# Kernel tuning notes

Measured on AMD Instinct MI355X. Metric: run time of the kernel, lower is better.

The kernel has to match this reference:

```python
import jax, jax.numpy as jnp
import numpy as np

DIM = 1024
NUM_HEADS = 16
HEAD_DIM = DIM // NUM_HEADS
SCALING = HEAD_DIM ** (-0.5)


def setup_inputs() -> dict:
    key = jax.random.key(0)
    ks = jax.random.split(key, 9)
    B, S = 2, 2048
    s = DIM ** -0.5  # ~ torch Linear init scale
    inp = {
        "x": jax.random.normal(ks[0], (B, S, DIM), dtype=jnp.float32),
        "wq": jax.random.uniform(ks[1], (DIM, DIM), jnp.float32, -s, s),
        "bq": jax.random.uniform(ks[2], (DIM,), jnp.float32, -s, s),
        "wk": jax.random.uniform(ks[3], (DIM, DIM), jnp.float32, -s, s),
        "bk": jax.random.uniform(ks[4], (DIM,), jnp.float32, -s, s),
        "wv": jax.random.uniform(ks[5], (DIM, DIM), jnp.float32, -s, s),
        "bv": jax.random.uniform(ks[6], (DIM,), jnp.float32, -s, s),
        "wo": jax.random.uniform(ks[7], (DIM, DIM), jnp.float32, -s, s),
        "bo": jax.random.uniform(ks[8], (DIM,), jnp.float32, -s, s),
    }
    return inp


def reference(x, wq, bq, wk, bk, wv, bv, wo, bo):
    B, S, D = x.shape
    # projections (weights stored [out,in] like torch Linear -> x @ W.T + b)
    q = (x @ wq.T + bq).reshape(B, S, NUM_HEADS, HEAD_DIM)
    k = (x @ wk.T + bk).reshape(B, S, NUM_HEADS, HEAD_DIM)
    v = (x @ wv.T + bv).reshape(B, S, NUM_HEADS, HEAD_DIM)
    # [B,H,S,S] scores, scaled
    scores = jnp.einsum("bqhd,bkhd->bhqk", q, k) * SCALING
    attn = jax.nn.softmax(scores, axis=-1)
    # dropout p=0.0 (eval): identity
    out = jnp.einsum("bhqk,bkhd->bqhd", attn, v).reshape(B, S, D)
    return out @ wo.T + bo
```

## Files before the change

kernel.cpp:

```cpp
#include <hip/hip_runtime.h>

#define DIM 1024
#define NHEADS 16
#define HDIM 64
#define BATCH 2
#define SEQ 2048
#define MTOT (BATCH*SEQ)
#define QSCALE 0.18033688011112042f
#define XN ((size_t)MTOT*DIM)
#define WN ((size_t)DIM*DIM)

typedef __attribute__((ext_vector_type(8))) short short8;
typedef __attribute__((ext_vector_type(4))) float f32x4;
typedef __attribute__((ext_vector_type(16))) float f32x16;
typedef __attribute__((ext_vector_type(2))) int int2v;

static __device__ __forceinline__ unsigned short bf16rne(float f) {
    unsigned u = __builtin_bit_cast(unsigned, f);
    return (unsigned short)((u + 0x7fffu + ((u >> 16) & 1u)) >> 16);
}

static __device__ __forceinline__ void gld16(const void* g, void* l) {
    __builtin_amdgcn_global_load_lds((const __attribute__((address_space(1))) void*)g,
                                     (__attribute__((address_space(3))) void*)l, 16, 0, 0);
}

__global__ __launch_bounds__(256)
void prep(const float* __restrict__ x, const float* __restrict__ wq, const float* __restrict__ wk,
          const float* __restrict__ wv, const float* __restrict__ wo, unsigned short* __restrict__ dst)
{
    const size_t i = ((size_t)blockIdx.x*256 + threadIdx.x)*8;
    const float* s; size_t o;
    if (i < XN)           { s = x;  o = i; }
    else if (i < XN+WN)   { s = wq; o = i - XN; }
    else if (i < XN+2*WN) { s = wk; o = i - XN - WN; }
    else if (i < XN+3*WN) { s = wv; o = i - XN - 2*WN; }
    else                  { s = wo; o = i - XN - 3*WN; }
    float4 a = *(const float4*)(s + o);
    float4 b = *(const float4*)(s + o + 4);
    uint4 w;
    w.x = (unsigned)bf16rne(a.x) | ((unsigned)bf16rne(a.y) << 16);
    w.y = (unsigned)bf16rne(a.z) | ((unsigned)bf16rne(a.w) << 16);
    w.z = (unsigned)bf16rne(b.x) | ((unsigned)bf16rne(b.y) << 16);
    w.w = (unsigned)bf16rne(b.z) | ((unsigned)bf16rne(b.w) << 16);
    *(uint4*)&dst[i] = w;
}

__global__ __launch_bounds__(256)
void gemm_qkv(const unsigned short* __restrict__ A,
              const unsigned short* __restrict__ W0, const unsigned short* __restrict__ W1,
              const unsigned short* __restrict__ W2,
              const float* __restrict__ b0, const float* __restrict__ b1, const float* __restrict__ b2,
              unsigned short* __restrict__ o0, unsigned short* __restrict__ o1, unsigned short* __restrict__ o2)
{
    __shared__ __align__(16) unsigned short As[2][4096];
    __shared__ __align__(16) unsigned short Bs[2][4096];
    const int t = threadIdx.x, wid = t >> 6, lane = t & 63;
    const int lr = lane & 15, lg = lane >> 4;
    const int bid = blockIdx.y * 24 + blockIdx.x;
    const int swz = (bid & 7) * 96 + (bid >> 3);
    const int sx = swz % 24, sy = swz / 24;
    const int widx = sx >> 3;
    const int n0 = (sx & 7) << 7;
    const int m0 = sy << 7;
    const unsigned short* W = widx == 0 ? W0 : (widx == 1 ? W1 : W2);
    const float* bias        = widx == 0 ? b0 : (widx == 1 ? b1 : b2);
    const float scale        = widx == 0 ? QSCALE : 1.0f;
    unsigned short* out      = widx == 0 ? o0 : (widx == 1 ? o1 : o2);

    const int wm = wid >> 1, wn = wid & 1;
    const int f0 = 2*wid, f1 = f0 + 1;
    const unsigned short* Ag0 = A + (size_t)(m0 + f0*16 + lr)*DIM + lg*8;
    const unsigned short* Ag1 = A + (size_t)(m0 + f1*16 + lr)*DIM + lg*8;
    const unsigned short* Bg0 = W + (size_t)(n0 + f0*16 + lr)*DIM + lg*8;
    const unsigned short* Bg1 = W + (size_t)(n0 + f1*16 + lr)*DIM + lg*8;

    f32x4 acc[4][4] = {};

    gld16(Ag0, &As[0][f0*512]); gld16(Ag1, &As[0][f1*512]);
    gld16(Bg0, &Bs[0][f0*512]); gld16(Bg1, &Bs[0][f1*512]);

    for (int it = 0; it < DIM/32; ++it) {
        __syncthreads();
        {
            const int nbf = (it+1)&1; const int ko = ((it+1)&31)*32;
            gld16(Ag0 + ko, &As[nbf][f0*512]); gld16(Ag1 + ko, &As[nbf][f1*512]);
            gld16(Bg0 + ko, &Bs[nbf][f0*512]); gld16(Bg1 + ko, &Bs[nbf][f1*512]);
        }
        const int cb = it & 1;
        short8 af[4], bf[4];
        #pragma unroll
        for (int i = 0; i < 4; ++i) af[i] = *(const short8*)&As[cb][(wm*4+i)*512 + lane*8];
        #pragma unroll
        for (int i = 0; i < 4; ++i) bf[i] = *(const short8*)&Bs[cb][(wn*4+i)*512 + lane*8];
        __builtin_amdgcn_s_setprio(1);
        #pragma unroll
        for (int mb = 0; mb < 4; ++mb)
            #pragma unroll
            for (int nb = 0; nb < 4; ++nb)
                acc[mb][nb] = __builtin_amdgcn_mfma_f32_16x16x32_bf16(af[mb], bf[nb], acc[mb][nb], 0, 0, 0);
        __builtin_amdgcn_s_setprio(0);
    }

    #pragma unroll
    for (int nb = 0; nb < 4; ++nb) {
        const int col = n0 + wn*64 + nb*16 + lr;
        const float bv = bias[col];
        #pragma unroll
        for (int mb = 0; mb < 4; ++mb) {
            #pragma unroll
            for (int j = 0; j < 4; ++j) {
                const int row = m0 + wm*64 + mb*16 + lg*4 + j;
                out[(size_t)row*DIM + col] = bf16rne((acc[mb][nb][j] + bv) * scale);
            }
        }
    }
}

__global__ __launch_bounds__(256)
void gemm_o(const unsigned short* __restrict__ A, const unsigned short* __restrict__ W,
            const float* __restrict__ bias, float* __restrict__ fo)
{
    __shared__ __align__(16) unsigned short As[2][2048];
    __shared__ __align__(16) unsigned short Bs[2][4096];
    const int t = threadIdx.x, wid = t >> 6, lane = t & 63;
    const int lr = lane & 15, lg = lane >> 4;
    const int bid = blockIdx.y * 8 + blockIdx.x;
    const int swz = (bid & 7) * 64 + (bid >> 3);
    const int n0 = (swz & 7) << 7;
    const int m0 = (swz >> 3) << 6;
    const int wm = wid >> 1, wn = wid & 1;

    const int fa = wid;
    const int g0 = 2*wid, g1 = g0 + 1;
    const unsigned short* Ag  = A + (size_t)(m0 + fa*16 + lr)*DIM + lg*8;
    const unsigned short* Bg0 = W + (size_t)(n0 + g0*16 + lr)*DIM + lg*8;
    const unsigned short* Bg1 = W + (size_t)(n0 + g1*16 + lr)*DIM + lg*8;

    f32x4 acc[2][4] = {};

    gld16(Ag, &As[0][fa*512]);
    gld16(Bg0, &Bs[0][g0*512]); gld16(Bg1, &Bs[0][g1*512]);

    for (int it = 0; it < DIM/32; ++it) {
        __syncthreads();
        {
            const int nbf = (it+1)&1; const int ko = ((it+1)&31)*32;
            gld16(Ag + ko, &As[nbf][fa*512]);
            gld16(Bg0 + ko, &Bs[nbf][g0*512]); gld16(Bg1 + ko, &Bs[nbf][g1*512]);
        }
        const int cb = it & 1;
        short8 af[2], bf[4];
        #pragma unroll
        for (int i = 0; i < 2; ++i) af[i] = *(const short8*)&As[cb][(wm*2+i)*512 + lane*8];
        #pragma unroll
        for (int i = 0; i < 4; ++i) bf[i] = *(const short8*)&Bs[cb][(wn*4+i)*512 + lane*8];
        __builtin_amdgcn_s_setprio(1);
        #pragma unroll
        for (int mb = 0; mb < 2; ++mb)
            #pragma unroll
            for (int nb = 0; nb < 4; ++nb)
                acc[mb][nb] = __builtin_amdgcn_mfma_f32_16x16x32_bf16(af[mb], bf[nb], acc[mb][nb], 0, 0, 0);
        __builtin_amdgcn_s_setprio(0);
    }

    #pragma unroll
    for (int nb = 0; nb < 4; ++nb) {
        const int col = n0 + wn*64 + nb*16 + lr;
        const float bv = bias[col];
        #pragma unroll
        for (int mb = 0; mb < 2; ++mb) {
            #pragma unroll
            for (int j = 0; j < 4; ++j) {
                const int row = m0 + wm*32 + mb*16 + lg*4 + j;
                fo[(size_t)row*DIM + col] = acc[mb][nb][j] + bv;
            }
        }
    }
}

__global__ __launch_bounds__(256)
void transpose_v(const unsigned short* __restrict__ V, unsigned short* __restrict__ Vt)
{
    __shared__ unsigned short tile[64][66];
    const int t  = threadIdx.x;
    const int st = blockIdx.x;
    const int bh = blockIdx.y;
    const int b = bh >> 4, h = bh & 15;
    const int sr = t >> 3;
    const int dc = (t & 7) * 8;

    #pragma unroll
    for (int r = 0; r < 2; ++r) {
        const int s = r*32 + sr;
        short8 v = *(const short8*)(V + (size_t)(b*SEQ + st*64 + s)*DIM + h*HDIM + dc);
        #pragma unroll
        for (int e = 0; e < 8; ++e) tile[s][dc + e] = (unsigned short)v[e];
    }
    __syncthreads();
    #pragma unroll
    for (int r = 0; r < 2; ++r) {
        const int d = r*32 + sr;
        short8 ov;
        #pragma unroll
        for (int e = 0; e < 8; ++e) ov[e] = (short)tile[dc + e][d];
        *(short8*)(Vt + (size_t)bh*HDIM*SEQ + (size_t)d*SEQ + st*64 + dc) = ov;
    }
}

__global__ __launch_bounds__(256)
void attn_mfma2(const unsigned short* __restrict__ Q, const unsigned short* __restrict__ Kg,
                const unsigned short* __restrict__ Vt, unsigned short* __restrict__ O)
{
    __shared__ __align__(16) unsigned short Ks[2][4096];
    __shared__ __align__(16) unsigned short Vs[2][4096];
    const int t = threadIdx.x, wid = t >> 6, lane = t & 63;
    const int l31 = lane & 31, h = lane >> 5;
    const int bid = blockIdx.y * 16 + blockIdx.x;
    const int swz = (bid & 7) * 64 + (bid >> 3);
    const int qt = swz & 15, bh = swz >> 4;
    const int b = bh >> 4, hh = bh & 15;
    const size_t qkbase = (size_t)b*SEQ*DIM + (size_t)hh*HDIM;
    const unsigned short* Qb = Q + qkbase;
    const unsigned short* Kb = Kg + qkbase;
    const unsigned short* Vb = Vt + (size_t)bh*HDIM*SEQ;
    unsigned short*       Ob = O + qkbase;
    const int q0 = qt*128 + wid*32;

    short8 qf[4];
    #pragma unroll
    for (int ds = 0; ds < 4; ++ds)
        qf[ds] = *(const short8*)&Qb[(size_t)(q0 + l31)*DIM + ds*16 + h*8];

    const int f0 = 2*wid, f1 = f0 + 1;
    const unsigned short* Kg0 = &Kb[(size_t)((f0>>2)*32 + l31)*DIM + (f0&3)*16 + h*8];
    const unsigned short* Kg1 = &Kb[(size_t)((f1>>2)*32 + l31)*DIM + (f1&3)*16 + h*8];
    const unsigned short* Vg0 = &Vb[(size_t)((f0>>2)*32 + l31)*SEQ + (f0&3)*16 + h*8];
    const unsigned short* Vg1 = &Vb[(size_t)((f1>>2)*32 + l31)*SEQ + (f1&3)*16 + h*8];

    f32x16 ctx0 = {}, ctx1 = {};
    float lsum = 0.0f;

    gld16(Kg0, &Ks[0][f0*512]); gld16(Kg1, &Ks[0][f1*512]);
    gld16(Vg0, &Vs[0][f0*512]); gld16(Vg1, &Vs[0][f1*512]);

    for (int kt = 0; kt < SEQ/64; ++kt) {
        __syncthreads();
        {
            const int nbf = (kt+1)&1;
            const int ktn = (kt+1) & (SEQ/64 - 1);
            const size_t koK = (size_t)ktn * 64 * DIM;
            const size_t koV = (size_t)ktn * 64;
            gld16(Kg0 + koK, &Ks[nbf][f0*512]); gld16(Kg1 + koK, &Ks[nbf][f1*512]);
            gld16(Vg0 + koV, &Vs[nbf][f0*512]); gld16(Vg1 + koV, &Vs[nbf][f1*512]);
        }
        const int cb = kt & 1;

        f32x16 s0 = {}, s1 = {};
        __builtin_amdgcn_s_setprio(1);
        #pragma unroll
        for (int ds = 0; ds < 4; ++ds) {
            short8 kf0 = *(const short8*)&Ks[cb][ds*512 + lane*8];
            short8 kf1 = *(const short8*)&Ks[cb][(4+ds)*512 + lane*8];
            s0 = __builtin_amdgcn_mfma_f32_32x32x16_bf16(kf0, qf[ds], s0, 0, 0, 0);
            s1 = __builtin_amdgcn_mfma_f32_32x32x16_bf16(kf1, qf[ds], s1, 0, 0, 0);
        }
        __builtin_amdgcn_s_setprio(0);

        float rsum = 0.0f;
        unsigned pw[2][4][2];
        #pragma unroll
        for (int r1 = 0; r1 < 4; ++r1)
            #pragma unroll
            for (int tt = 0; tt < 2; ++tt) {
                float pa_ = __builtin_amdgcn_exp2f(s0[4*r1+2*tt]);
                float pb_ = __builtin_amdgcn_exp2f(s0[4*r1+2*tt+1]);
                float pc_ = __builtin_amdgcn_exp2f(s1[4*r1+2*tt]);
                float pd_ = __builtin_amdgcn_exp2f(s1[4*r1+2*tt+1]);
                rsum += (pa_ + pb_) + (pc_ + pd_);
                unsigned w0, w1;
                asm("v_cvt_pk_bf16_f32 %0, %1, %2" : "=v"(w0) : "v"(pa_), "v"(pb_));
                asm("v_cvt_pk_bf16_f32 %0, %1, %2" : "=v"(w1) : "v"(pc_), "v"(pd_));
                pw[0][r1][tt] = w0;
                pw[1][r1][tt] = w1;
            }
        rsum += __shfl_xor(rsum, 32);
        lsum += rsum;

        short8 pa4[4];
        #pragma unroll
        for (int ss = 0; ss < 4; ++ss) {
            union { short8 s8; unsigned u[4]; } pu;
            #pragma unroll
            for (int tt = 0; tt < 2; ++tt) {
                int2v sw = __builtin_amdgcn_permlane32_swap(
                    (int)pw[ss>>1][2*(ss&1)][tt], (int)pw[ss>>1][2*(ss&1)+1][tt], false, false);
                pu.u[tt]     = (unsigned)sw[0];
                pu.u[2 + tt] = (unsigned)sw[1];
            }
            pa4[ss] = pu.s8;
        }

        __builtin_amdgcn_s_setprio(1);
        #pragma unroll
        for (int ss = 0; ss < 4; ++ss) {
            short8 vf0 = *(const short8*)&Vs[cb][ss*512 + lane*8];
            short8 vf1 = *(const short8*)&Vs[cb][(4+ss)*512 + lane*8];
            ctx0 = __builtin_amdgcn_mfma_f32_32x32x16_bf16(pa4[ss], vf0, ctx0, 0, 0, 0);
            ctx1 = __builtin_amdgcn_mfma_f32_32x32x16_bf16(pa4[ss], vf1, ctx1, 0, 0, 0);
        }
        __builtin_amdgcn_s_setprio(0);
    }

    const float linv = 1.0f / lsum;
    #pragma unroll
    for (int r = 0; r < 16; ++r) {
        const int qrow = (r&3) + 8*(r>>2) + 4*h;
        const float nm = __shfl(linv, qrow);
        unsigned short* p = &Ob[(size_t)(q0 + qrow)*DIM + l31];
        p[0]  = bf16rne(ctx0[r] * nm);
        p[32] = bf16rne(ctx1[r] * nm);
    }
}

extern "C" void kernel_launch(void* const* d_in, const int* in_sizes, int n_in,
                              void* d_out, int out_size, void* d_ws, size_t ws_size,
                              hipStream_t stream) {
    const float* x  = (const float*)d_in[0];
    const float* wq = (const float*)d_in[1];
    const float* bq = (const float*)d_in[2];
    const float* wk = (const float*)d_in[3];
    const float* bk = (const float*)d_in[4];
    const float* wv = (const float*)d_in[5];
    const float* bv = (const float*)d_in[6];
    const float* wo = (const float*)d_in[7];
    const float* bo = (const float*)d_in[8];
    float* out = (float*)d_out;

    unsigned short* Xb  = (unsigned short*)d_ws;
    unsigned short* Wqb = Xb  + XN;
    unsigned short* Wkb = Wqb + WN;
    unsigned short* Wvb = Wkb + WN;
    unsigned short* Wob = Wvb + WN;
    unsigned short* Qb  = Wob + WN;
    unsigned short* Kb  = Qb  + XN;
    unsigned short* Vb  = Kb  + XN;
    unsigned short* Vtb = Vb  + XN;
    unsigned short* Cb  = Vb;

    prep<<<4096, 256, 0, stream>>>(x, wq, wk, wv, wo, Xb);

    gemm_qkv<<<dim3(24, 32), 256, 0, stream>>>(Xb, Wqb, Wkb, Wvb, bq, bk, bv, Qb, Kb, Vb);

    transpose_v<<<dim3(SEQ/64, BATCH*NHEADS), 256, 0, stream>>>(Vb, Vtb);
    attn_mfma2<<<dim3(SEQ/128, BATCH*NHEADS), 256, 0, stream>>>(Qb, Kb, Vtb, Cb);

    gemm_o<<<dim3(8, 64), 256, 0, stream>>>(Cb, Wob, bo, out);
}
```

Before: 151.5 us.

## Fuse V transpose into QKV GEMM epilogue and software-pipeline attention over two key tiles

The QKV projection GEMM now writes V directly in transposed per-head layout, so the separate transpose_v kernel and its extra read/write pass over V go away. The attention kernel processes two 64-key tiles per loop iteration using a 4-deep LDS ring. The QK^T MFMAs of the second tile are interleaved with the PV MFMAs of the first, so exp/softmax work can overlap matrix-core work. The cost is doubled LDS use, which may lower occupancy, plus scattered 8-byte stores in the V epilogue.

```diff
diff --git a/kernel.cpp b/kernel.cpp
--- a/kernel.cpp
+++ b/kernel.cpp
@@ -23,6 +23,10 @@
 static __device__ __forceinline__ void gld16(const void* g, void* l) {
     __builtin_amdgcn_global_load_lds((const __attribute__((address_space(1))) void*)g,
                                      (__attribute__((address_space(3))) void*)l, 16, 0, 0);
+}
+
+static __device__ __forceinline__ f32x16 mfma32(short8 a, short8 b, f32x16 c) {
+    return __builtin_amdgcn_mfma_f32_32x32x16_bf16(a, b, c, 0, 0, 0);
 }
 
 __global__ __launch_bounds__(256)
@@ -102,16 +106,35 @@
         __builtin_amdgcn_s_setprio(0);
     }
 
-    #pragma unroll
-    for (int nb = 0; nb < 4; ++nb) {
-        const int col = n0 + wn*64 + nb*16 + lr;
-        const float bv = bias[col];
-        #pragma unroll
-        for (int mb = 0; mb < 4; ++mb) {
-            #pragma unroll
-            for (int j = 0; j < 4; ++j) {
-                const int row = m0 + wm*64 + mb*16 + lg*4 + j;
-                out[(size_t)row*DIM + col] = bf16rne((acc[mb][nb][j] + bv) * scale);
+    if (widx == 2) {
+        const int bb  = m0 >> 11;
+        const int sb  = (m0 & (SEQ-1)) + wm*64;
+        #pragma unroll
+        for (int nb = 0; nb < 4; ++nb) {
+            const int col = n0 + wn*64 + nb*16 + lr;
+            const int hh = col >> 6, dd = col & 63;
+            const float bv = bias[col];
+            unsigned short* vt = out + ((size_t)(bb*NHEADS + hh)*HDIM + dd)*SEQ;
+            #pragma unroll
+            for (int mb = 0; mb < 4; ++mb) {
+                const int srow = sb + mb*16 + lg*4;
+                unsigned w0 = (unsigned)bf16rne(acc[mb][nb][0]+bv) | ((unsigned)bf16rne(acc[mb][nb][1]+bv) << 16);
+                unsigned w1 = (unsigned)bf16rne(acc[mb][nb][2]+bv) | ((unsigned)bf16rne(acc[mb][nb][3]+bv) << 16);
+                *(uint2*)&vt[srow] = make_uint2(w0, w1);
+            }
+        }
+    } else {
+        #pragma unroll
+        for (int nb = 0; nb < 4; ++nb) {
+            const int col = n0 + wn*64 + nb*16 + lr;
+            const float bv = bias[col];
+            #pragma unroll
+            for (int mb = 0; mb < 4; ++mb) {
+                #pragma unroll
+                for (int j = 0; j < 4; ++j) {
+                    const int row = m0 + wm*64 + mb*16 + lg*4 + j;
+                    out[(size_t)row*DIM + col] = bf16rne((acc[mb][nb][j] + bv) * scale);
+                }
             }
         }
     }
@@ -179,41 +202,48 @@
     }
 }
 
-__global__ __launch_bounds__(256)
-void transpose_v(const unsigned short* __restrict__ V, unsigned short* __restrict__ Vt)
-{
-    __shared__ unsigned short tile[64][66];
-    const int t  = threadIdx.x;
-    const int st = blockIdx.x;
-    const int bh = blockIdx.y;
-    const int b = bh >> 4, h = bh & 15;
-    const int sr = t >> 3;
-    const int dc = (t & 7) * 8;
-
-    #pragma unroll
-    for (int r = 0; r < 2; ++r) {
-        const int s = r*32 + sr;
-        short8 v = *(const short8*)(V + (size_t)(b*SEQ + st*64 + s)*DIM + h*HDIM + dc);
-        #pragma unroll
-        for (int e = 0; e < 8; ++e) tile[s][dc + e] = (unsigned short)v[e];
-    }
-    __syncthreads();
-    #pragma unroll
-    for (int r = 0; r < 2; ++r) {
-        const int d = r*32 + sr;
-        short8 ov;
-        #pragma unroll
-        for (int e = 0; e < 8; ++e) ov[e] = (short)tile[dc + e][d];
-        *(short8*)(Vt + (size_t)bh*HDIM*SEQ + (size_t)d*SEQ + st*64 + dc) = ov;
-    }
+struct PA { short8 p[4]; };
+
+static __device__ __forceinline__ PA softmax_pack(const f32x16& s0, const f32x16& s1, float& lsum) {
+    float rsum = 0.f;
+    unsigned pw0[4][2], pw1[4][2];
+    #pragma unroll
+    for (int r1 = 0; r1 < 4; ++r1)
+        #pragma unroll
+        for (int tt = 0; tt < 2; ++tt) {
+            float pa_ = __builtin_amdgcn_exp2f(s0[4*r1+2*tt]);
+            float pb_ = __builtin_amdgcn_exp2f(s0[4*r1+2*tt+1]);
+            float pc_ = __builtin_amdgcn_exp2f(s1[4*r1+2*tt]);
+            float pd_ = __builtin_amdgcn_exp2f(s1[4*r1+2*tt+1]);
+            rsum += (pa_ + pb_) + (pc_ + pd_);
+            asm("v_cvt_pk_bf16_f32 %0, %1, %2" : "=v"(pw0[r1][tt]) : "v"(pa_), "v"(pb_));
+            asm("v_cvt_pk_bf16_f32 %0, %1, %2" : "=v"(pw1[r1][tt]) : "v"(pc_), "v"(pd_));
+        }
+    rsum += __shfl_xor(rsum, 32);
+    lsum += rsum;
+    PA r;
+    #pragma unroll
+    for (int ss = 0; ss < 4; ++ss) {
+        union { short8 s8; unsigned u[4]; } pu;
+        #pragma unroll
+        for (int tt = 0; tt < 2; ++tt) {
+            const unsigned a = (ss >> 1) ? pw1[2*(ss&1)][tt]   : pw0[2*(ss&1)][tt];
+            const unsigned b = (ss >> 1) ? pw1[2*(ss&1)+1][tt] : pw0[2*(ss&1)+1][tt];
+            int2v sw = __builtin_amdgcn_permlane32_swap((int)a, (int)b, false, false);
+            pu.u[tt]     = (unsigned)sw[0];
+            pu.u[2 + tt] = (unsigned)sw[1];
+        }
+        r.p[ss] = pu.s8;
+    }
+    return r;
 }
 
 __global__ __launch_bounds__(256)
 void attn_mfma2(const unsigned short* __restrict__ Q, const unsigned short* __restrict__ Kg,
                 const unsigned short* __restrict__ Vt, unsigned short* __restrict__ O)
 {
-    __shared__ __align__(16) unsigned short Ks[2][4096];
-    __shared__ __align__(16) unsigned short Vs[2][4096];
+    __shared__ __align__(16) unsigned short Ks[4][4096];
+    __shared__ __align__(16) unsigned short Vs[4][4096];
     const int t = threadIdx.x, wid = t >> 6, lane = t & 63;
     const int l31 = lane & 31, h = lane >> 5;
     const int bid = blockIdx.y * 16 + blockIdx.x;
@@ -238,76 +268,65 @@
     const unsigned short* Vg0 = &Vb[(size_t)((f0>>2)*32 + l31)*SEQ + (f0&3)*16 + h*8];
     const unsigned short* Vg1 = &Vb[(size_t)((f1>>2)*32 + l31)*SEQ + (f1&3)*16 + h*8];
 
+    auto stage = [&](int tn) {
+        const size_t koK = (size_t)tn * 64 * DIM;
+        const size_t koV = (size_t)tn * 64;
+        const int bb = tn & 3;
+        gld16(Kg0 + koK, &Ks[bb][f0*512]); gld16(Kg1 + koK, &Ks[bb][f1*512]);
+        gld16(Vg0 + koV, &Vs[bb][f0*512]); gld16(Vg1 + koV, &Vs[bb][f1*512]);
+    };
+
     f32x16 ctx0 = {}, ctx1 = {};
     float lsum = 0.0f;
 
-    gld16(Kg0, &Ks[0][f0*512]); gld16(Kg1, &Ks[0][f1*512]);
-    gld16(Vg0, &Vs[0][f0*512]); gld16(Vg1, &Vs[0][f1*512]);
-
-    for (int kt = 0; kt < SEQ/64; ++kt) {
+    stage(0); stage(1);
+
+    for (int w = 0; w < SEQ/128; ++w) {
+        const int t0 = 2*w;
+        const int ba = t0 & 3, bb2 = (t0+1) & 3;
         __syncthreads();
-        {
-            const int nbf = (kt+1)&1;
-            const int ktn = (kt+1) & (SEQ/64 - 1);
-            const size_t koK = (size_t)ktn * 64 * DIM;
-            const size_t koV = (size_t)ktn * 64;
-            gld16(Kg0 + koK, &Ks[nbf][f0*512]); gld16(Kg1 + koK, &Ks[nbf][f1*512]);
-            gld16(Vg0 + koV, &Vs[nbf][f0*512]); gld16(Vg1 + koV, &Vs[nbf][f1*512]);
-        }
-        const int cb = kt & 1;
-
-        f32x16 s0 = {}, s1 = {};
+        if (w + 1 < SEQ/128) { stage(t0+2); stage(t0+3); }
+
+        f32x16 s0a = {}, s1a = {};
         __builtin_amdgcn_s_setprio(1);
         #pragma unroll
         for (int ds = 0; ds < 4; ++ds) {
-            short8 kf0 = *(const short8*)&Ks[cb][ds*512 + lane*8];
-            short8 kf1 = *(const short8*)&Ks[cb][(4+ds)*512 + lane*8];
-            s0 = __builtin_amdgcn_mfma_f32_32x32x16_bf16(kf0, qf[ds], s0, 0, 0, 0);
-            s1 = __builtin_amdgcn_mfma_f32_32x32x16_bf16(kf1, qf[ds], s1, 0, 0, 0);
-        }
-        __builtin_amdgcn_s_setprio(0);
-
-        float rsum = 0.0f;
-        unsigned pw[2][4][2];
-        #pragma unroll
-        for (int r1 = 0; r1 < 4; ++r1)
-            #pragma unroll
-            for (int tt = 0; tt < 2; ++tt) {
-                float pa_ = __builtin_amdgcn_exp2f(s0[4*r1+2*tt]);
-                float pb_ = __builtin_amdgcn_exp2f(s0[4*r1+2*tt+1]);
-                float pc_ = __builtin_amdgcn_exp2f(s1[4*r1+2*tt]);
-                float pd_ = __builtin_amdgcn_exp2f(s1[4*r1+2*tt+1]);
-                rsum += (pa_ + pb_) + (pc_ + pd_);
-                unsigned w0, w1;
-                asm("v_cvt_pk_bf16_f32 %0, %1, %2" : "=v"(w0) : "v"(pa_), "v"(pb_));
-                asm("v_cvt_pk_bf16_f32 %0, %1, %2" : "=v"(w1) : "v"(pc_), "v"(pd_));
-                pw[0][r1][tt] = w0;
-                pw[1][r1][tt] = w1;
-            }
-        rsum += __shfl_xor(rsum, 32);
-        lsum += rsum;
-
-        short8 pa4[4];
+            short8 kf0 = *(const short8*)&Ks[ba][ds*512 + lane*8];
+            short8 kf1 = *(const short8*)&Ks[ba][(4+ds)*512 + lane*8];
+            s0a = mfma32(kf0, qf[ds], s0a);
+            s1a = mfma32(kf1, qf[ds], s1a);
+        }
+        __builtin_amdgcn_s_setprio(0);
+
+        PA pa = softmax_pack(s0a, s1a, lsum);
+
+        f32x16 s0b = {}, s1b = {};
+        __builtin_amdgcn_s_setprio(1);
+        #pragma unroll
+        for (int ds = 0; ds < 4; ++ds) {
+            short8 kf0 = *(const short8*)&Ks[bb2][ds*512 + lane*8];
+            short8 kf1 = *(const short8*)&Ks[bb2][(4+ds)*512 + lane*8];
+            s0b = mfma32(kf0, qf[ds], s0b);
+            s1b = mfma32(kf1, qf[ds], s1b);
+        }
         #pragma unroll
         for (int ss = 0; ss < 4; ++ss) {
-            union { short8 s8; unsigned u[4]; } pu;
-            #pragma unroll
-            for (int tt = 0; tt < 2; ++tt) {
-                int2v sw = __builtin_amdgcn_permlane32_swap(
-                    (int)pw[ss>>1][2*(ss&1)][tt], (int)pw[ss>>1][2*(ss&1)+1][tt], false, false);
-                pu.u[tt]     = (unsigned)sw[0];
-                pu.u[2 + tt] = (unsigned)sw[1];
-            }
-            pa4[ss] = pu.s8;
-        }
+            short8 vf0 = *(const short8*)&Vs[ba][ss*512 + lane*8];
+            short8 vf1 = *(const short8*)&Vs[ba][(4+ss)*512 + lane*8];
+            ctx0 = mfma32(pa.p[ss], vf0, ctx0);
+            ctx1 = mfma32(pa.p[ss], vf1, ctx1);
+        }
+        __builtin_amdgcn_s_setprio(0);
+
+        PA pb = softmax_pack(s0b, s1b, lsum);
 
         __builtin_amdgcn_s_setprio(1);
         #pragma unroll
         for (int ss = 0; ss < 4; ++ss) {
-            short8 vf0 = *(const short8*)&Vs[cb][ss*512 + lane*8];
-            short8 vf1 = *(const short8*)&Vs[cb][(4+ss)*512 + lane*8];
-            ctx0 = __builtin_amdgcn_mfma_f32_32x32x16_bf16(pa4[ss], vf0, ctx0, 0, 0, 0);
-            ctx1 = __builtin_amdgcn_mfma_f32_32x32x16_bf16(pa4[ss], vf1, ctx1, 0, 0, 0);
+            short8 vf0 = *(const short8*)&Vs[bb2][ss*512 + lane*8];
+            short8 vf1 = *(const short8*)&Vs[bb2][(4+ss)*512 + lane*8];
+            ctx0 = mfma32(pb.p[ss], vf0, ctx0);
+            ctx1 = mfma32(pb.p[ss], vf1, ctx1);
         }
         __builtin_amdgcn_s_setprio(0);
     }
@@ -344,15 +363,13 @@
     unsigned short* Wob = Wvb + WN;
     unsigned short* Qb  = Wob + WN;
     unsigned short* Kb  = Qb  + XN;
-    unsigned short* Vb  = Kb  + XN;
-    unsigned short* Vtb = Vb  + XN;
-    unsigned short* Cb  = Vb;
+    unsigned short* Cb  = Kb  + XN;
+    unsigned short* Vtb = Cb  + XN;
 
     prep<<<4096, 256, 0, stream>>>(x, wq, wk, wv, wo, Xb);
 
-    gemm_qkv<<<dim3(24, 32), 256, 0, stream>>>(Xb, Wqb, Wkb, Wvb, bq, bk, bv, Qb, Kb, Vb);
-
-    transpose_v<<<dim3(SEQ/64, BATCH*NHEADS), 256, 0, stream>>>(Vb, Vtb);
+    gemm_qkv<<<dim3(24, 32), 256, 0, stream>>>(Xb, Wqb, Wkb, Wvb, bq, bk, bv, Qb, Kb, Vtb);
+
     attn_mfma2<<<dim3(SEQ/128, BATCH*NHEADS), 256, 0, stream>>>(Qb, Kb, Vtb, Cb);
 
     gemm_o<<<dim3(8, 64), 256, 0, stream>>>(Cb, Wob, bo, out);
```

After: 160.3 us. +5.8%, slower.
